# Kernel tuning notes

Measured on AMD Instinct MI355X. Metric: run time of the kernel, lower is better.

The kernel has to match this reference:

```python
import jax, jax.numpy as jnp
import numpy as np
from jax import lax

# --- RPN config (eval / TEST path) ---
ASPECT = (0.5, 1.0, 2.0)
SCALE = (8.0, 16.0, 32.0)
STRIDE = 16
N_ANCHORS = len(ASPECT) * len(SCALE)  # 9
PRE_NMS = 6000
POST_NMS = 300
NMS_THRESH = 0.7
MIN_SIZE = 16.0
NEG = jnp.float32(-1e9)


def conv2d(x, w, b, pad):
    y = lax.conv_general_dilated(x, w, (1, 1), [(pad, pad), (pad, pad)],
                                 dimension_numbers=('NCHW', 'OIHW', 'NCHW'))
    return y + b[None, :, None, None]


def make_anchors(h, w):
    asp = jnp.array(ASPECT, jnp.float32)
    sc = jnp.array(SCALE, jnp.float32)
    size = float(STRIDE * STRIDE)
    ws = (jnp.sqrt(size / asp)[:, None] * sc[None, :]).reshape(-1)  # (A,)
    hs = (jnp.sqrt(size * asp)[:, None] * sc[None, :]).reshape(-1)
    c = (STRIDE - 1) / 2.0
    base = jnp.stack([c - 0.5 * (ws - 1), c - 0.5 * (hs - 1),
                      c + 0.5 * (ws - 1), c + 0.5 * (hs - 1)], axis=-1)  # (A,4)
    sx = jnp.arange(w, dtype=jnp.float32) * STRIDE
    sy = jnp.arange(h, dtype=jnp.float32) * STRIDE
    shift_x, shift_y = jnp.meshgrid(sx, sy)  # (h,w)
    shifts = jnp.stack([shift_x, shift_y, shift_x, shift_y], axis=-1)  # (h,w,4)
    return (shifts[:, :, None, :] + base[None, None]).reshape(-1, 4)  # (h*w*A,4)


def decode_boxes(anchors, deltas):
    wa = anchors[..., 2] - anchors[..., 0] + 1.0
    ha = anchors[..., 3] - anchors[..., 1] + 1.0
    cxa = anchors[..., 0] + 0.5 * wa
    cya = anchors[..., 1] + 0.5 * ha
    cx = deltas[..., 0] * wa + cxa
    cy = deltas[..., 1] * ha + cya
    pw = jnp.exp(deltas[..., 2]) * wa
    ph = jnp.exp(deltas[..., 3]) * ha
    return jnp.stack([cx - 0.5 * pw, cy - 0.5 * ph,
                      cx + 0.5 * pw, cy + 0.5 * ph], axis=-1)


def iou_one_many(box, boxes):
    x1 = jnp.maximum(box[0], boxes[:, 0])
    y1 = jnp.maximum(box[1], boxes[:, 1])
    x2 = jnp.minimum(box[2], boxes[:, 2])
    y2 = jnp.minimum(box[3], boxes[:, 3])
    inter = jnp.maximum(0.0, x2 - x1 + 1.0) * jnp.maximum(0.0, y2 - y1 + 1.0)
    a0 = (box[2] - box[0] + 1.0) * (box[3] - box[1] + 1.0)
    a1 = (boxes[:, 2] - boxes[:, 0] + 1.0) * (boxes[:, 3] - boxes[:, 1] + 1.0)
    return inter / (a0 + a1 - inter)


def nms_keep(boxes, scores):
    # boxes: (PRE,4) sorted by score desc; returns POST_NMS kept indices
    n = boxes.shape[0]

    def body(i, carry):
        valid, keep = carry
        s = jnp.where(valid, scores, NEG)
        j = jnp.argmax(s).astype(jnp.int32)
        keep = keep.at[i].set(j)
        iou = iou_one_many(boxes[j], boxes)
        valid = valid & (iou <= NMS_THRESH)
        valid = valid.at[j].set(False)
        return valid, keep

    _, keep = lax.fori_loop(0, POST_NMS, body,
                            (jnp.ones(n, bool), jnp.zeros(POST_NMS, jnp.int32)))
    return keep


def rpn_forward(input, im_info, w_feat, b_feat, w_cls, b_cls, w_reg, b_reg):
    feat = jax.nn.relu(conv2d(input, w_feat, b_feat, 1))  # (B,512,h,w)
    cls = conv2d(feat, w_cls, b_cls, 0)                    # (B,2A,h,w)
    B, _, h, w = cls.shape
    prob = jax.nn.softmax(cls.reshape(B, N_ANCHORS, 2, h, w), axis=2)
    fg = prob[:, :, 1]                                     # (B,A,h,w)
    scores = fg.transpose(0, 2, 3, 1).reshape(B, h * w * N_ANCHORS)
    reg = conv2d(feat, w_reg, b_reg, 0)                    # (B,4A,h,w)
    deltas = reg.transpose(0, 2, 3, 1).reshape(B, h * w * N_ANCHORS, 4)

    anchors = make_anchors(h, w)                           # (K,4)
    boxes = decode_boxes(anchors[None], deltas)            # (B,K,4)

    # clip to image
    im_h = im_info[:, 0][:, None]
    im_w = im_info[:, 1][:, None]
    x1 = jnp.clip(boxes[..., 0], 0.0, im_w - 1.0)
    y1 = jnp.clip(boxes[..., 1], 0.0, im_h - 1.0)
    x2 = jnp.clip(boxes[..., 2], 0.0, im_w - 1.0)
    y2 = jnp.clip(boxes[..., 3], 0.0, im_h - 1.0)
    boxes = jnp.stack([x1, y1, x2, y2], axis=-1)

    # min-size filter (mask scores instead of dropping rows)
    ms = MIN_SIZE * im_info[:, 2][:, None]
    ok = ((x2 - x1 + 1.0) >= ms) & ((y2 - y1 + 1.0) >= ms)
    scores = jnp.where(ok, scores, NEG)

    top_scores, order = lax.top_k(scores, PRE_NMS)         # (B,PRE)
    boxes_sorted = jnp.take_along_axis(boxes, order[..., None], axis=1)
    keep = jax.vmap(nms_keep)(boxes_sorted, top_scores)    # (B,POST)
    rois_boxes = jnp.take_along_axis(boxes_sorted, keep[..., None], axis=1)
    bidx = jnp.broadcast_to(jnp.arange(B, dtype=boxes.dtype)[:, None, None],
                            (B, POST_NMS, 1))
    return jnp.concatenate([bidx, rois_boxes], axis=-1)    # (B,POST,5)


def setup_inputs() -> dict:
    key = jax.random.key(0)
    ks = jax.random.split(key, 8)
    B, C, H, W = 8, 512, 64, 64
    inp = {
        'input': jax.random.normal(ks[0], (B, C, H, W), jnp.float32),
        'gt_box': jnp.zeros((B, 20, 5), jnp.float32),
        'im_info': jnp.tile(jnp.array([[1024.0, 1024.0, 1.0]], jnp.float32), (B, 1)),
        'w_feat': jax.random.normal(ks[1], (512, 512, 3, 3), jnp.float32) * 0.01,
        'b_feat': jnp.zeros((512,), jnp.float32),
        'w_cls': jax.random.normal(ks[2], (2 * N_ANCHORS, 512, 1, 1), jnp.float32) * 0.01,
        'b_cls': jnp.zeros((2 * N_ANCHORS,), jnp.float32),
        'w_reg': jax.random.normal(ks[3], (4 * N_ANCHORS, 512, 1, 1), jnp.float32) * 0.01,
        'b_reg': jnp.zeros((4 * N_ANCHORS,), jnp.float32),
    }
    return inp


def reference(input, gt_box, im_info, w_feat, b_feat, w_cls, b_cls, w_reg, b_reg):
    # eval-mode RPN: module returns (0, 0, rois); we return rois
    return rpn_forward(input, im_info, w_feat, b_feat, w_cls, b_cls, w_reg, b_reg)
```

## Files before the change

### kernel.cpp

```cpp
#include <hip/hip_runtime.h>
#include <hip/hip_bf16.h>
#include <stdint.h>

#define HW      64
#define CIN     512
#define KOUT    512
#define BATCH   8
#define NANCH   9
#define NBOX    (HW*HW*NANCH)
#define PRE_NMS 6000
#define POST_NMS 300
#define SORT_N  8192

__global__ __launch_bounds__(256)
void transpose_w(const float* __restrict__ w, float* __restrict__ wt) {
    __shared__ float t[32][33];
    const int jt = blockIdx.x * 32, kt = blockIdx.y * 32;
    const int c  = threadIdx.x & 31, r8 = threadIdx.x >> 5;
#pragma unroll
    for (int p = 0; p < 4; ++p) {
        int kl = r8 + p * 8;
        t[kl][c] = w[(size_t)(kt + kl) * 4608 + jt + c];
    }
    __syncthreads();
#pragma unroll
    for (int p = 0; p < 4; ++p) {
        int jl = r8 + p * 8;
        wt[(size_t)(jt + jl) * 512 + kt + c] = t[c][jl];
    }
}

__global__ __launch_bounds__(256)
void conv3x3_relu(const float* __restrict__ in, const float* __restrict__ wt,
                  const float* __restrict__ bias, float* __restrict__ feat) {
    __shared__ float s_in[2][8 * 3 * 68 + 4];

    const int tid = threadIdx.x;
    const int k0  = blockIdx.x * 64;
    const int y   = blockIdx.y;
    const int b   = blockIdx.z;
    const int x   = tid & 63;
    const int kw  = __builtin_amdgcn_readfirstlane(tid >> 6);
    const int kb  = k0 + kw * 16;

    int in_lds[2]; int in_goff[2]; bool in_act[2], in_ok[2];
#pragma unroll
    for (int s = 0; s < 2; ++s) {
        int q   = tid + 256 * s;
        bool a  = (q < 384);
        int qq  = a ? q : 0;
        int ci  = qq / 48, rem = qq % 48;
        int r   = rem >> 4, c4 = rem & 15;
        int gy  = y - 1 + r;
        in_act[s] = a;
        in_ok[s]  = a && ((unsigned)gy < 64u);
        int gyc   = gy < 0 ? 0 : (gy > 63 ? 63 : gy);
        in_lds[s] = 4 + (ci * 3 + r) * 68 + 4 * c4;
        in_goff[s] = ((b * 512 + ci) * 64 + gyc) * 64 + 4 * c4;
    }

    for (int i = tid; i < 2 * (8 * 3 * 68 + 4); i += 256) ((float*)s_in)[i] = 0.0f;
    __syncthreads();

    float4 pin[2];
    const float4 z4 = make_float4(0.f, 0.f, 0.f, 0.f);
    auto prefetch = [&](int cc8) {
#pragma unroll
        for (int s = 0; s < 2; ++s)
            pin[s] = in_ok[s] ? *(const float4*)&in[in_goff[s] + cc8 * 32768] : z4;
    };
    prefetch(0);

    float acc[16];
#pragma unroll
    for (int k = 0; k < 16; ++k) acc[k] = 0.0f;

    for (int cc8 = 0; cc8 < 64; ++cc8) {
        float* SIN = &s_in[cc8 & 1][0];

#pragma unroll
        for (int s = 0; s < 2; ++s)
            if (in_act[s]) *(float4*)&SIN[in_lds[s]] = pin[s];
        __syncthreads();
        if (cc8 < 63) prefetch(cc8 + 1);

#pragma unroll
        for (int ci = 0; ci < 8; ++ci) {
#pragma unroll
            for (int dy = 0; dy < 3; ++dy) {
                const float* rp = &SIN[4 + (ci * 3 + dy) * 68];
                float ivv[3];
                ivv[0] = rp[x - 1];
                ivv[1] = rp[x];
                ivv[2] = rp[x + 1];
#pragma unroll
                for (int dx = 0; dx < 3; ++dx) {
                    const float* wp = &wt[(size_t)((cc8 * 8 + ci) * 9 + dy * 3 + dx) * 512 + kb];
                    float4 wA = *(const float4*)(wp);
                    float4 wB = *(const float4*)(wp + 4);
                    float4 wC = *(const float4*)(wp + 8);
                    float4 wD = *(const float4*)(wp + 12);
                    float wv[16] = {wA.x, wA.y, wA.z, wA.w, wB.x, wB.y, wB.z, wB.w,
                                    wC.x, wC.y, wC.z, wC.w, wD.x, wD.y, wD.z, wD.w};
                    float f = ivv[dx];
#pragma unroll
                    for (int k = 0; k < 16; ++k)
                        acc[k] = fmaf(f, wv[k], acc[k]);
                }
            }
        }
    }
#pragma unroll
    for (int k = 0; k < 16; ++k) {
        float v = fmaxf(acc[k] + bias[kb + k], 0.0f);
        feat[(((size_t)b * KOUT + kb + k) * HW + y) * HW + x] = v;
    }
}

__global__ __launch_bounds__(128, 2)
void heads(const float* __restrict__ feat,
           const float* __restrict__ wcls, const float* __restrict__ bcls,
           const float* __restrict__ wreg, const float* __restrict__ breg,
           const float* __restrict__ iminfo,
           unsigned long long* __restrict__ keys, float4* __restrict__ pbox) {
    __shared__ float s_w[128 * 56];

    const int tid = threadIdx.x;
    const int pix = blockIdx.x * 128 + tid;
    const int b   = pix >> 12;
    const int rem = pix & 4095;
    const int y   = rem >> 6;
    const int x   = rem & 63;

    float acc[54];
#pragma unroll
    for (int j = 0; j < 54; ++j) acc[j] = 0.0f;

    for (int cc = 0; cc < 512; cc += 128) {
        __syncthreads();
        for (int i = tid; i < 128 * 56; i += 128) {
            int cl = i / 56; int j = i % 56;
            float v = 0.0f;
            if (j < 18)      v = wcls[(size_t)j * 512 + cc + cl];
            else if (j < 54) v = wreg[(size_t)(j - 18) * 512 + cc + cl];
            s_w[i] = v;
        }
        __syncthreads();
#pragma unroll 4
        for (int c2 = 0; c2 < 128; ++c2) {
            float f = feat[(((size_t)b * 512 + cc + c2) * 64 + y) * 64 + x];
            const float* wr = &s_w[c2 * 56];
#pragma unroll
            for (int j4 = 0; j4 < 13; ++j4) {
                float4 w4 = *(const float4*)&wr[4 * j4];
                acc[4 * j4 + 0] = fmaf(f, w4.x, acc[4 * j4 + 0]);
                acc[4 * j4 + 1] = fmaf(f, w4.y, acc[4 * j4 + 1]);
                acc[4 * j4 + 2] = fmaf(f, w4.z, acc[4 * j4 + 2]);
                acc[4 * j4 + 3] = fmaf(f, w4.w, acc[4 * j4 + 3]);
            }
            float4 wt4 = *(const float4*)&wr[52];
            acc[52] = fmaf(f, wt4.x, acc[52]);
            acc[53] = fmaf(f, wt4.y, acc[53]);
        }
    }

    const float im_h = iminfo[b * 3 + 0];
    const float im_w = iminfo[b * 3 + 1];
    const float ms   = 16.0f * iminfo[b * 3 + 2];
    const float ASP[3] = {0.5f, 1.0f, 2.0f};
    const float SCL[3] = {8.0f, 16.0f, 32.0f};

#pragma unroll
    for (int a = 0; a < 9; ++a) {
        float c0 = acc[2 * a]     + bcls[2 * a];
        float c1 = acc[2 * a + 1] + bcls[2 * a + 1];
        float m  = fmaxf(c0, c1);
        float e0 = expf(c0 - m), e1 = expf(c1 - m);
        float fg = e1 / (e0 + e1);

        float d0 = acc[18 + 4 * a + 0] + breg[4 * a + 0];
        float d1 = acc[18 + 4 * a + 1] + breg[4 * a + 1];
        float d2 = acc[18 + 4 * a + 2] + breg[4 * a + 2];
        float d3 = acc[18 + 4 * a + 3] + breg[4 * a + 3];

        int ai = a / 3, si = a % 3;
        float wsz = sqrtf(256.0f / ASP[ai]) * SCL[si];
        float hsz = sqrtf(256.0f * ASP[ai]) * SCL[si];
        float sx = (float)x * 16.0f, sy = (float)y * 16.0f;
        float x1a = sx + (7.5f - 0.5f * (wsz - 1.0f));
        float y1a = sy + (7.5f - 0.5f * (hsz - 1.0f));
        float x2a = sx + (7.5f + 0.5f * (wsz - 1.0f));
        float y2a = sy + (7.5f + 0.5f * (hsz - 1.0f));

        float wa = x2a - x1a + 1.0f, ha = y2a - y1a + 1.0f;
        float cxa = x1a + 0.5f * wa, cya = y1a + 0.5f * ha;
        float cx = d0 * wa + cxa, cy = d1 * ha + cya;
        float pw = expf(d2) * wa, ph = expf(d3) * ha;
        float bx1 = cx - 0.5f * pw, by1 = cy - 0.5f * ph;
        float bx2 = cx + 0.5f * pw, by2 = cy + 0.5f * ph;

        bx1 = fminf(fmaxf(bx1, 0.0f), im_w - 1.0f);
        by1 = fminf(fmaxf(by1, 0.0f), im_h - 1.0f);
        bx2 = fminf(fmaxf(bx2, 0.0f), im_w - 1.0f);
        by2 = fminf(fmaxf(by2, 0.0f), im_h - 1.0f);

        bool ok = (bx2 - bx1 + 1.0f >= ms) && (by2 - by1 + 1.0f >= ms);
        float s = ok ? fg : -1e9f;

        unsigned u = __float_as_uint(s);
        u = (u & 0x80000000u) ? ~u : (u | 0x80000000u);
        int idx = (y * 64 + x) * 9 + a;
        keys[(size_t)b * NBOX + idx] =
            ((unsigned long long)u << 32) | (unsigned)(~(unsigned)idx);
        pbox[(size_t)b * NBOX + idx] = make_float4(bx1, by1, bx2, by2);
    }
}

__global__ __launch_bounds__(1024)
void select_sort(const unsigned long long* __restrict__ keys,
                 const float4* __restrict__ pbox,
                 float4* __restrict__ sorted) {
    __shared__ unsigned long long sbuf[SORT_N];
    __shared__ unsigned hist[16][256];
    __shared__ unsigned sh_prefix, sh_remaining, sh_counter;

    const int tid = threadIdx.x;
    const int b   = blockIdx.x;
    const int wv  = tid >> 6;
    const unsigned long long* kb = keys + (size_t)b * NBOX;

    if (tid == 0) { sh_prefix = 0u; sh_remaining = PRE_NMS; sh_counter = 0u; }

    for (int p = 3; p >= 0; --p) {
        for (int i = tid; i < 16 * 256; i += 1024) ((unsigned*)hist)[i] = 0u;
        __syncthreads();
        unsigned prefix = sh_prefix;
        unsigned pmask  = (p == 3) ? 0u : (0xFFFFFFFFu << (8 * (p + 1)));
        for (int i = tid; i < NBOX; i += 1024) {
            unsigned u = (unsigned)(kb[i] >> 32);
            if ((u & pmask) == prefix)
                atomicAdd(&hist[wv][(u >> (8 * p)) & 255], 1u);
        }
        __syncthreads();
        if (tid < 256) {
            unsigned s = 0;
#pragma unroll
            for (int w2 = 0; w2 < 16; ++w2) s += hist[w2][tid];
            hist[0][tid] = s;
        }
        __syncthreads();
        if (tid == 0) {
            unsigned rem = sh_remaining;
            int v = 255;
            for (; v > 0; --v) {
                unsigned c = hist[0][v];
                if (rem <= c) break;
                rem -= c;
            }
            sh_prefix    = prefix | ((unsigned)v << (8 * p));
            sh_remaining = rem;
        }
        __syncthreads();
    }
    const unsigned thr = sh_prefix;

    for (int i = tid; i < NBOX; i += 1024) {
        unsigned long long k = kb[i];
        bool act = ((unsigned)(k >> 32) >= thr);
        unsigned long long bal = __ballot(act);
        if (act) {
            int lane   = tid & 63;
            int leader = __ffsll(bal) - 1;
            unsigned base = 0;
            if (lane == leader) base = atomicAdd(&sh_counter, (unsigned)__popcll(bal));
            base = __shfl(base, leader);
            unsigned off = (unsigned)__popcll(bal & ((1ull << lane) - 1ull));
            unsigned pos2 = base + off;
            if (pos2 < SORT_N) sbuf[pos2] = k;
        }
    }
    __syncthreads();
    unsigned n = sh_counter; if (n > SORT_N) n = SORT_N;
    for (int i = (int)n + tid; i < SORT_N; i += 1024) sbuf[i] = 0ull;
    __syncthreads();

    for (int k = 2; k <= SORT_N; k <<= 1) {
        for (int j = k >> 1; j > 0; j >>= 1) {
            for (int t = tid; t < SORT_N / 2; t += 1024) {
                int i  = ((t & ~(j - 1)) << 1) | (t & (j - 1));
                int ix = i | j;
                bool up = ((i & k) == 0);
                unsigned long long a = sbuf[i], c = sbuf[ix];
                bool sw = up ? (a < c) : (a > c);
                if (sw) { sbuf[i] = c; sbuf[ix] = a; }
            }
            __syncthreads();
        }
    }

    for (int i = tid; i < PRE_NMS; i += 1024) {
        unsigned idx = ~((unsigned)sbuf[i]);
        sorted[(size_t)b * PRE_NMS + i] = pbox[(size_t)b * NBOX + idx];
    }
}

__global__ __launch_bounds__(512, 2)
void nms(const float4* __restrict__ sorted, float* __restrict__ out) {
    __shared__ unsigned long long vmask[94];
    __shared__ int sh_j;

    const int tid = threadIdx.x;
    const int b   = blockIdx.x;
    const float4* sb = sorted + (size_t)b * PRE_NMS;

    float4 bx[12]; float ar[12];
#pragma unroll
    for (int s = 0; s < 12; ++s) {
        int i = tid + 512 * s;
        if (i < PRE_NMS) {
            float4 v = sb[i];
            bx[s] = v;
            ar[s] = (v.z - v.x + 1.0f) * (v.w - v.y + 1.0f);
        } else {
            bx[s] = make_float4(0.f, 0.f, 0.f, 0.f);
            ar[s] = 1.0f;
        }
    }
    if (tid < 94) vmask[tid] = (tid < 93) ? ~0ull : ((1ull << 48) - 1ull);
    __syncthreads();

    for (int it = 0; it < POST_NMS; ++it) {
        if (tid < 64) {
            unsigned long long w0 = vmask[tid];
            unsigned long long w1 = (tid < 30) ? vmask[tid + 64] : 0ull;
            int cand = w0 ? (tid * 64 + __ffsll(w0) - 1)
                          : (w1 ? ((tid + 64) * 64 + __ffsll(w1) - 1) : 0x7FFFFFFF);
#pragma unroll
            for (int off = 32; off > 0; off >>= 1) {
                int o = __shfl_xor(cand, off);
                cand = (o < cand) ? o : cand;
            }
            if (tid == 0) sh_j = (cand == 0x7FFFFFFF) ? 0 : cand;
        }
        __syncthreads();
        int j = sh_j;
        float4 jb = sb[j];
        if (tid == 0) {
            float* o = out + ((size_t)b * POST_NMS + it) * 5;
            o[0] = (float)b; o[1] = jb.x; o[2] = jb.y; o[3] = jb.z; o[4] = jb.w;
        }
        float ja = (jb.z - jb.x + 1.0f) * (jb.w - jb.y + 1.0f);
#pragma unroll
        for (int s = 0; s < 12; ++s) {
            int i = tid + 512 * s;
            if (i < PRE_NMS && ((vmask[i >> 6] >> (i & 63)) & 1ull)) {
                float xx1 = fmaxf(jb.x, bx[s].x);
                float yy1 = fmaxf(jb.y, bx[s].y);
                float xx2 = fminf(jb.z, bx[s].z);
                float yy2 = fminf(jb.w, bx[s].w);
                float inter = fmaxf(0.0f, xx2 - xx1 + 1.0f) *
                              fmaxf(0.0f, yy2 - yy1 + 1.0f);
                float iou = inter / (ja + ar[s] - inter);
                if (iou > 0.7f)
                    atomicAnd(&vmask[i >> 6], ~(1ull << (i & 63)));
            }
        }
        __syncthreads();
    }
}

extern "C" void kernel_launch(void* const* d_in, const int* in_sizes, int n_in,
                              void* d_out, int out_size, void* d_ws, size_t ws_size,
                              hipStream_t stream) {
    (void)in_sizes; (void)n_in; (void)out_size; (void)ws_size;
    const float* input  = (const float*)d_in[0];
    const float* iminfo = (const float*)d_in[2];
    const float* wfeat  = (const float*)d_in[3];
    const float* bfeat  = (const float*)d_in[4];
    const float* wcls   = (const float*)d_in[5];
    const float* bcls   = (const float*)d_in[6];
    const float* wreg   = (const float*)d_in[7];
    const float* breg   = (const float*)d_in[8];
    float* out = (float*)d_out;

    char* ws = (char*)d_ws;
    float*               feat   = (float*)ws;
    float*               wt     = (float*)(ws + 67108864);
    unsigned long long*  keys   = (unsigned long long*)(ws + 67108864);
    float4*              pbox   = (float4*)(ws + 67108864 + 2359296);
    float4*              sorted = (float4*)(ws + 67108864 + 2359296 + 4718592);

    transpose_w<<<dim3(144, 16), 256, 0, stream>>>(wfeat, wt);
    conv3x3_relu<<<dim3(8, 64, 8), 256, 0, stream>>>(input, wt, bfeat, feat);
    heads<<<dim3(256), 128, 0, stream>>>(feat, wcls, bcls, wreg, breg, iminfo, keys, pbox);
    select_sort<<<dim3(8), 1024, 0, stream>>>(keys, pbox, sorted);
    nms<<<dim3(8), 512, 0, stream>>>(sorted, out);
}
```

Before: 3.364 ms.

## Rewrite NMS as single-wave lane-owned bitmask loop; tweak conv occupancy attributes

```diff
diff --git a/kernel.cpp b/kernel.cpp
--- a/kernel.cpp
+++ b/kernel.cpp
@@ -30,7 +30,9 @@
     }
 }
 
-__global__ __launch_bounds__(256)
+__global__
+__attribute__((amdgpu_flat_work_group_size(256, 256)))
+__attribute__((amdgpu_waves_per_eu(2, 4)))
 void conv3x3_relu(const float* __restrict__ in, const float* __restrict__ wt,
                   const float* __restrict__ bias, float* __restrict__ feat) {
     __shared__ float s_in[2][8 * 3 * 68 + 4];
@@ -71,9 +73,10 @@
     };
     prefetch(0);
 
-    float acc[16];
-#pragma unroll
-    for (int k = 0; k < 16; ++k) acc[k] = 0.0f;
+    float a00 = 0.f, a01 = 0.f, a02 = 0.f, a03 = 0.f;
+    float a04 = 0.f, a05 = 0.f, a06 = 0.f, a07 = 0.f;
+    float a08 = 0.f, a09 = 0.f, a10 = 0.f, a11 = 0.f;
+    float a12 = 0.f, a13 = 0.f, a14 = 0.f, a15 = 0.f;
 
     for (int cc8 = 0; cc8 < 64; ++cc8) {
         float* SIN = &s_in[cc8 & 1][0];
@@ -89,10 +92,9 @@
 #pragma unroll
             for (int dy = 0; dy < 3; ++dy) {
                 const float* rp = &SIN[4 + (ci * 3 + dy) * 68];
-                float ivv[3];
-                ivv[0] = rp[x - 1];
-                ivv[1] = rp[x];
-                ivv[2] = rp[x + 1];
+                float iv0 = rp[x - 1];
+                float iv1 = rp[x];
+                float iv2 = rp[x + 1];
 #pragma unroll
                 for (int dx = 0; dx < 3; ++dx) {
                     const float* wp = &wt[(size_t)((cc8 * 8 + ci) * 9 + dy * 3 + dx) * 512 + kb];
@@ -100,19 +102,32 @@
                     float4 wB = *(const float4*)(wp + 4);
                     float4 wC = *(const float4*)(wp + 8);
                     float4 wD = *(const float4*)(wp + 12);
-                    float wv[16] = {wA.x, wA.y, wA.z, wA.w, wB.x, wB.y, wB.z, wB.w,
-                                    wC.x, wC.y, wC.z, wC.w, wD.x, wD.y, wD.z, wD.w};
-                    float f = ivv[dx];
-#pragma unroll
-                    for (int k = 0; k < 16; ++k)
-                        acc[k] = fmaf(f, wv[k], acc[k]);
+                    float f = (dx == 0) ? iv0 : (dx == 1) ? iv1 : iv2;
+                    a00 = fmaf(f, wA.x, a00);
+                    a01 = fmaf(f, wA.y, a01);
+                    a02 = fmaf(f, wA.z, a02);
+                    a03 = fmaf(f, wA.w, a03);
+                    a04 = fmaf(f, wB.x, a04);
+                    a05 = fmaf(f, wB.y, a05);
+                    a06 = fmaf(f, wB.z, a06);
+                    a07 = fmaf(f, wB.w, a07);
+                    a08 = fmaf(f, wC.x, a08);
+                    a09 = fmaf(f, wC.y, a09);
+                    a10 = fmaf(f, wC.z, a10);
+                    a11 = fmaf(f, wC.w, a11);
+                    a12 = fmaf(f, wD.x, a12);
+                    a13 = fmaf(f, wD.y, a13);
+                    a14 = fmaf(f, wD.z, a14);
+                    a15 = fmaf(f, wD.w, a15);
                 }
             }
         }
     }
+    float accv[16] = {a00, a01, a02, a03, a04, a05, a06, a07,
+                      a08, a09, a10, a11, a12, a13, a14, a15};
 #pragma unroll
     for (int k = 0; k < 16; ++k) {
-        float v = fmaxf(acc[k] + bias[kb + k], 0.0f);
+        float v = fmaxf(accv[k] + bias[kb + k], 0.0f);
         feat[(((size_t)b * KOUT + kb + k) * HW + y) * HW + x] = v;
     }
 }
@@ -304,68 +319,68 @@
     }
 }
 
-__global__ __launch_bounds__(512, 2)
+__global__ __launch_bounds__(64)
 void nms(const float4* __restrict__ sorted, float* __restrict__ out) {
-    __shared__ unsigned long long vmask[94];
-    __shared__ int sh_j;
-
-    const int tid = threadIdx.x;
-    const int b   = blockIdx.x;
+    __shared__ float4 sbx[94 * 65];
+
+    const int lane = threadIdx.x;
+    const int b    = blockIdx.x;
     const float4* sb = sorted + (size_t)b * PRE_NMS;
 
-    float4 bx[12]; float ar[12];
-#pragma unroll
-    for (int s = 0; s < 12; ++s) {
-        int i = tid + 512 * s;
-        if (i < PRE_NMS) {
-            float4 v = sb[i];
-            bx[s] = v;
-            ar[s] = (v.z - v.x + 1.0f) * (v.w - v.y + 1.0f);
-        } else {
-            bx[s] = make_float4(0.f, 0.f, 0.f, 0.f);
-            ar[s] = 1.0f;
-        }
-    }
-    if (tid < 94) vmask[tid] = (tid < 93) ? ~0ull : ((1ull << 48) - 1ull);
+    for (int i = lane; i < PRE_NMS; i += 64)
+        sbx[(i >> 6) * 65 + (i & 63)] = sb[i];
     __syncthreads();
 
+    unsigned long long m0 = ~0ull;
+    unsigned           m1 = (lane < 48) ? 0x3FFFFFFFu
+                                        : 0x1FFFFFFFu;
+
     for (int it = 0; it < POST_NMS; ++it) {
-        if (tid < 64) {
-            unsigned long long w0 = vmask[tid];
-            unsigned long long w1 = (tid < 30) ? vmask[tid + 64] : 0ull;
-            int cand = w0 ? (tid * 64 + __ffsll(w0) - 1)
-                          : (w1 ? ((tid + 64) * 64 + __ffsll(w1) - 1) : 0x7FFFFFFF);
-#pragma unroll
-            for (int off = 32; off > 0; off >>= 1) {
-                int o = __shfl_xor(cand, off);
-                cand = (o < cand) ? o : cand;
-            }
-            if (tid == 0) sh_j = (cand == 0x7FFFFFFF) ? 0 : cand;
-        }
-        __syncthreads();
-        int j = sh_j;
-        float4 jb = sb[j];
-        if (tid == 0) {
+        int cand;
+        if (m0)      cand = (__ffsll(m0) - 1) * 64 + lane;
+        else if (m1) cand = (64 + __ffs(m1) - 1) * 64 + lane;
+        else         cand = 0x7FFFFFFF;
+#pragma unroll
+        for (int off = 32; off > 0; off >>= 1) {
+            int o = __shfl_xor(cand, off);
+            cand = (o < cand) ? o : cand;
+        }
+        int j = (cand == 0x7FFFFFFF) ? 0 : cand;
+        float4 jb = sbx[(j >> 6) * 65 + (j & 63)];
+        if (lane == 0) {
             float* o = out + ((size_t)b * POST_NMS + it) * 5;
             o[0] = (float)b; o[1] = jb.x; o[2] = jb.y; o[3] = jb.z; o[4] = jb.w;
         }
         float ja = (jb.z - jb.x + 1.0f) * (jb.w - jb.y + 1.0f);
-#pragma unroll
-        for (int s = 0; s < 12; ++s) {
-            int i = tid + 512 * s;
-            if (i < PRE_NMS && ((vmask[i >> 6] >> (i & 63)) & 1ull)) {
-                float xx1 = fmaxf(jb.x, bx[s].x);
-                float yy1 = fmaxf(jb.y, bx[s].y);
-                float xx2 = fminf(jb.z, bx[s].z);
-                float yy2 = fminf(jb.w, bx[s].w);
-                float inter = fmaxf(0.0f, xx2 - xx1 + 1.0f) *
-                              fmaxf(0.0f, yy2 - yy1 + 1.0f);
-                float iou = inter / (ja + ar[s] - inter);
-                if (iou > 0.7f)
-                    atomicAnd(&vmask[i >> 6], ~(1ull << (i & 63)));
-            }
-        }
-        __syncthreads();
+
+        unsigned long long t0 = m0;
+        while (t0) {
+            int s = __ffsll(t0) - 1; t0 &= t0 - 1;
+            float4 v = sbx[s * 65 + lane];
+            float xx1 = fmaxf(jb.x, v.x);
+            float yy1 = fmaxf(jb.y, v.y);
+            float xx2 = fminf(jb.z, v.z);
+            float yy2 = fminf(jb.w, v.w);
+            float inter = fmaxf(0.0f, xx2 - xx1 + 1.0f) *
+                          fmaxf(0.0f, yy2 - yy1 + 1.0f);
+            float ar = (v.z - v.x + 1.0f) * (v.w - v.y + 1.0f);
+            float iou = inter / (ja + ar - inter);
+            if (iou > 0.7f) m0 &= ~(1ull << s);
+        }
+        unsigned t1 = m1;
+        while (t1) {
+            int s = __ffs(t1) - 1; t1 &= t1 - 1;
+            float4 v = sbx[(64 + s) * 65 + lane];
+            float xx1 = fmaxf(jb.x, v.x);
+            float yy1 = fmaxf(jb.y, v.y);
+            float xx2 = fminf(jb.z, v.z);
+            float yy2 = fminf(jb.w, v.w);
+            float inter = fmaxf(0.0f, xx2 - xx1 + 1.0f) *
+                          fmaxf(0.0f, yy2 - yy1 + 1.0f);
+            float ar = (v.z - v.x + 1.0f) * (v.w - v.y + 1.0f);
+            float iou = inter / (ja + ar - inter);
+            if (iou > 0.7f) m1 &= ~(1u << s);
+        }
     }
 }
 
@@ -394,5 +409,5 @@
     conv3x3_relu<<<dim3(8, 64, 8), 256, 0, stream>>>(input, wt, bfeat, feat);
     heads<<<dim3(256), 128, 0, stream>>>(feat, wcls, bcls, wreg, breg, iminfo, keys, pbox);
     select_sort<<<dim3(8), 1024, 0, stream>>>(keys, pbox, sorted);
-    nms<<<dim3(8), 512, 0, stream>>>(sorted, out);
-}
+    nms<<<dim3(8), 64, 0, stream>>>(sorted, out);
+}
```

After: 7.257 ms. 2.16x slower.
